# Performance work log

Hardware: AMD Instinct MI355X
Metric: run time of the kernel (lower is better)

The kernel has to match this reference:

```python
import jax, jax.numpy as jnp
import numpy as np

DIM = 2240; HEADS = 20; HD = 112
B = 1; F = 8; H = 16; W = 28; S = F * H * W; ENC = 300
HID = int(3.0 * DIM)  # 6720
EPS_LN = 1e-6; EPS_RMS = 1e-5


def setup_inputs():
    ks = iter(jax.random.split(jax.random.key(0), 64))
    nrm = lambda shape, s=1.0: jax.random.normal(next(ks), shape, jnp.float32) * s
    wsc = 0.02
    inp = dict(
        hidden_states=nrm((B, S, DIM)),
        encoder_hidden_states=nrm((B, ENC, DIM)),
        timestep=nrm((B, 6 * DIM), 0.1),
        freqs_cos=nrm((1, S, 1, HD)),
        freqs_sin=nrm((1, S, 1, HD)),
        scale_shift_table=nrm((6, DIM), 1.0 / np.sqrt(DIM)),
    )
    for p in ("a1", "a2"):
        inp[p + "_qw"] = nrm((DIM, DIM), wsc); inp[p + "_qb"] = jnp.zeros((DIM,), jnp.float32)
        inp[p + "_kw"] = nrm((DIM, DIM), wsc); inp[p + "_kb"] = jnp.zeros((DIM,), jnp.float32)
        inp[p + "_vw"] = nrm((DIM, DIM), wsc); inp[p + "_vb"] = jnp.zeros((DIM,), jnp.float32)
        inp[p + "_nq"] = jnp.ones((DIM,), jnp.float32)
        inp[p + "_nk"] = jnp.ones((DIM,), jnp.float32)
        inp[p + "_ow"] = nrm((DIM, DIM), wsc); inp[p + "_ob"] = jnp.zeros((DIM,), jnp.float32)
    inp["ff_inv_w"] = nrm((1, 1, DIM, 2 * HID), wsc)
    inp["ff_inv_b"] = jnp.zeros((2 * HID,), jnp.float32)
    inp["ff_depth_w"] = nrm((3, 3, 1, 2 * HID), wsc)
    inp["ff_depth_b"] = jnp.zeros((2 * HID,), jnp.float32)
    inp["ff_point_w"] = nrm((1, 1, HID, DIM), wsc)
    inp["ff_temp_w"] = nrm((3, 1, DIM, DIM), wsc)
    inp["frames"] = F; inp["height"] = H; inp["width"] = W
    return inp


def _ln(x):  # LayerNorm, no affine (elementwise_affine=False)
    m = jnp.mean(x, -1, keepdims=True)
    v = jnp.mean((x - m) ** 2, -1, keepdims=True)
    return (x - m) * jax.lax.rsqrt(v + EPS_LN)


def _rms(x, w):  # rms_norm_across_heads on full inner dim
    return x * jax.lax.rsqrt(jnp.mean(x * x, -1, keepdims=True) + EPS_RMS) * w


def _rope(x, cos, sin):  # interleaved rotary as in SanaLinearAttnProcessor3_0
    x1, x2 = x[..., 0::2], x[..., 1::2]
    c, s = cos[..., 0::2], sin[..., 1::2]
    out = jnp.stack([x1 * c - x2 * s, x1 * s + x2 * c], axis=-1)
    return out.reshape(x.shape)


def _conv(x, k, padding, groups=1):
    return jax.lax.conv_general_dilated(
        x, k, (1, 1), padding,
        dimension_numbers=("NHWC", "HWIO", "NHWC"),
        feature_group_count=groups)


def _linear_attn(x, qw, qb, kw, kb, vw, vb, nq, nk, ow, ob, cos, sin):
    b, s, _ = x.shape
    q = jax.nn.relu(_rms(x @ qw + qb, nq)).reshape(b, s, HEADS, HD)
    k = jax.nn.relu(_rms(x @ kw + kb, nk)).reshape(b, s, HEADS, HD)
    v = (x @ vw + vb).reshape(b, s, HEADS, HD)
    qr, kr = _rope(q, cos, sin), _rope(k, cos, sin)
    ksum = jnp.sum(k, axis=1)                             # [b,h,d] (un-rotated)
    denom = jnp.einsum("bhd,bshd->bsh", ksum, q) + 1e-15  # z^{-1}
    scores = jnp.einsum("bshe,bshd->bhed", v, kr)         # [b,h,dv,d]
    out = jnp.einsum("bhed,bshd->bshe", scores, qr) / denom[..., None]
    return out.reshape(b, s, HEADS * HD) @ ow + ob


def _cross_attn(x, enc, qw, qb, kw, kb, vw, vb, nq, nk, ow, ob):
    b, s, _ = x.shape; t = enc.shape[1]
    q = _rms(x @ qw + qb, nq).reshape(b, s, HEADS, HD)
    k = _rms(enc @ kw + kb, nk).reshape(b, t, HEADS, HD)
    v = (enc @ vw + vb).reshape(b, t, HEADS, HD)
    logits = jnp.einsum("bshd,bthd->bhst", q, k) / np.sqrt(HD).astype(np.float32)
    attn = jax.nn.softmax(logits, axis=-1)
    out = jnp.einsum("bhst,bthd->bshd", attn, v).reshape(b, s, HEADS * HD)
    return out @ ow + ob


def _ff(x, inv_w, inv_b, depth_w, depth_b, point_w, temp_w, f, h, w):
    b = x.shape[0]
    y = x.reshape(b * f, h, w, DIM)
    y = jax.nn.silu(_conv(y, inv_w, "SAME") + inv_b)
    y = _conv(y, depth_w, "SAME", groups=2 * HID) + depth_b
    a, g = y[..., :HID], y[..., HID:]
    y = _conv(a * jax.nn.silu(g), point_w, "SAME")        # [bf,h,w,DIM]
    yt = y.reshape(b, f, h * w, DIM)                      # conv over frames axis
    yt = yt + _conv(yt, temp_w, ((1, 1), (0, 0)))
    return yt.reshape(b, f, h, w, DIM)


def reference(hidden_states, encoder_hidden_states, timestep, freqs_cos, freqs_sin,
              scale_shift_table,
              a1_qw, a1_qb, a1_kw, a1_kb, a1_vw, a1_vb, a1_nq, a1_nk, a1_ow, a1_ob,
              a2_qw, a2_qb, a2_kw, a2_kb, a2_vw, a2_vb, a2_nq, a2_nk, a2_ow, a2_ob,
              ff_inv_w, ff_inv_b, ff_depth_w, ff_depth_b, ff_point_w, ff_temp_w,
              frames, height, width):
    b = hidden_states.shape[0]
    mods = scale_shift_table[None] + timestep.reshape(b, 6, DIM)
    sh_msa, sc_msa, g_msa, sh_mlp, sc_mlp, g_mlp = jnp.split(mods, 6, axis=1)
    nh = _ln(hidden_states) * (1 + sc_msa) + sh_msa
    attn = _linear_attn(nh, a1_qw, a1_qb, a1_kw, a1_kb, a1_vw, a1_vb,
                        a1_nq, a1_nk, a1_ow, a1_ob, freqs_cos, freqs_sin)
    x = hidden_states + g_msa * attn
    x = x + _cross_attn(x, encoder_hidden_states, a2_qw, a2_qb, a2_kw, a2_kb,
                        a2_vw, a2_vb, a2_nq, a2_nk, a2_ow, a2_ob)
    nh = _ln(x) * (1 + sc_mlp) + sh_mlp
    ff = _ff(nh.reshape(b, frames, height, width, DIM),
             ff_inv_w, ff_inv_b, ff_depth_w, ff_depth_b, ff_point_w, ff_temp_w,
             frames, height, width)
    x = x + g_mlp * ff.reshape(b, frames * height * width, DIM)
    return x
```

## Files before the change

kernel.cpp:

```cpp
#include <hip/hip_runtime.h>

#define DIMC 2240
#define STOK 3584
#define ENCT 300
#define NH   20
#define HDIM 112
#define HID1 6720
#define HID2 13440
#define DD   (2240*2240)
#define SD   (3584*2240)

typedef short bf16x8 __attribute__((ext_vector_type(8)));
typedef float f32x4  __attribute__((ext_vector_type(4)));

__device__ __forceinline__ unsigned short f2bf(float f){
  unsigned int u = __float_as_uint(f);
  u += 0x7fffu + ((u >> 16) & 1u);
  return (unsigned short)(u >> 16);
}
__device__ __forceinline__ float bf2f(unsigned short h){
  return __uint_as_float(((unsigned int)h) << 16);
}
__device__ __forceinline__ void gl_lds16(const unsigned short* g, unsigned short* l){
  __builtin_amdgcn_global_load_lds(
      (const __attribute__((address_space(1))) unsigned int*)(const void*)g,
      (__attribute__((address_space(3))) unsigned int*)(void*)l, 16, 0, 0);
}

__global__ void cvt_k(const float4* __restrict__ src, ushort4* __restrict__ dst, int n4){
  int i = blockIdx.x*256 + threadIdx.x;
  if (i < n4){
    float4 v = src[i];
    ushort4 o; o.x = f2bf(v.x); o.y = f2bf(v.y); o.z = f2bf(v.z); o.w = f2bf(v.w);
    dst[i] = o;
  }
}

__global__ __launch_bounds__(256) void cvt_t_k(const float* __restrict__ src,
    unsigned short* __restrict__ dst, int rows, int ldsrc, int c0, int nc){
  __shared__ float tile[32][33];
  const int tx = threadIdx.x & 31, ty = threadIdx.x >> 5;
  const int colBase = blockIdx.x*32;
  #pragma unroll
  for (int i = 0; i < 4; ++i){
    int rr = blockIdx.y*32 + ty + i*8;
    int cc = colBase + tx;
    tile[ty + i*8][tx] = (cc < nc) ? src[(size_t)rr*ldsrc + c0 + cc] : 0.f;
  }
  __syncthreads();
  #pragma unroll
  for (int i = 0; i < 4; ++i){
    int n = colBase + ty + i*8;
    int k = blockIdx.y*32 + tx;
    dst[(size_t)n*rows + k] = f2bf(tile[tx][ty + i*8]);
  }
}

__global__ void pack3_k(float* __restrict__ dst, const float* __restrict__ b0,
    const float* __restrict__ b1, const float* __restrict__ b2, int nslots){
  int i = blockIdx.x*256 + threadIdx.x;
  if (i >= nslots*2304) return;
  int slot = i / 2304, d = i - slot*2304;
  const float* src = (slot == 0) ? b0 : ((slot == 1) ? b1 : b2);
  dst[i] = (d < 2240) ? src[d] : 0.f;
}

__global__ void mods_k(const float* __restrict__ sst, const float* __restrict__ ts, float* __restrict__ mods){
  int i = blockIdx.x*256 + threadIdx.x;
  if (i < 6*DIMC) mods[i] = sst[i] + ts[i];
}

__global__ __launch_bounds__(256) void ln_mod_k(const float* __restrict__ x,
    const float* __restrict__ mods, int shj, int scj, unsigned short* __restrict__ out)
{
  const int s = blockIdx.x;
  const float* row = x + (size_t)s*DIMC;
  const float* sh = mods + shj*DIMC;
  const float* sc = mods + scj*DIMC;
  float sum = 0.f, sq = 0.f;
  for (int d = threadIdx.x; d < DIMC; d += 256){ float v = row[d]; sum += v; sq += v*v; }
  #pragma unroll
  for (int o = 32; o; o >>= 1){ sum += __shfl_down(sum, o); sq += __shfl_down(sq, o); }
  __shared__ float sA[4], sB[4];
  int w = threadIdx.x >> 6, l = threadIdx.x & 63;
  if (!l){ sA[w] = sum; sB[w] = sq; }
  __syncthreads();
  sum = sA[0]+sA[1]+sA[2]+sA[3];
  sq  = sB[0]+sB[1]+sB[2]+sB[3];
  float mean = sum * (1.f/DIMC);
  float rs = rsqrtf(sq*(1.f/DIMC) - mean*mean + 1e-6f);
  unsigned short* orow = out + (size_t)s*DIMC;
  for (int d = threadIdx.x; d < DIMC; d += 256){
    float v = (row[d]-mean)*rs*(1.f + sc[d]) + sh[d];
    orow[d] = f2bf(v);
  }
}

template<int RELU, int ROPE>
__global__ __launch_bounds__(256) void rms_bf_k(unsigned short* __restrict__ x, const float* __restrict__ nw,
    const float* __restrict__ cosb, const float* __restrict__ sinb, unsigned short* __restrict__ xr)
{
  const int s = blockIdx.x;
  unsigned short* row = x + (size_t)s*DIMC;
  float sq = 0.f;
  for (int d = threadIdx.x; d < DIMC; d += 256){ float v = bf2f(row[d]); sq += v*v; }
  #pragma unroll
  for (int o = 32; o; o >>= 1) sq += __shfl_down(sq, o);
  __shared__ float sB[4];
  int w = threadIdx.x >> 6, l = threadIdx.x & 63;
  if (!l) sB[w] = sq;
  __syncthreads();
  sq = sB[0]+sB[1]+sB[2]+sB[3];
  float rs = rsqrtf(sq*(1.f/DIMC) + 1e-5f);
  if constexpr (!ROPE){
    for (int d = threadIdx.x; d < DIMC; d += 256){
      float v = bf2f(row[d])*rs*nw[d];
      if (RELU) v = fmaxf(v, 0.f);
      row[d] = f2bf(v);
    }
  } else {
    for (int p = threadIdx.x; p < DIMC/2; p += 256){
      int d0 = 2*p, d1 = d0+1;
      float v0 = bf2f(row[d0])*rs*nw[d0];
      float v1 = bf2f(row[d1])*rs*nw[d1];
      if (RELU){ v0 = fmaxf(v0,0.f); v1 = fmaxf(v1,0.f); }
      row[d0] = f2bf(v0); row[d1] = f2bf(v1);
      int j0 = d0 % HDIM;
      float c  = cosb[(size_t)s*HDIM + j0];
      float sn = sinb[(size_t)s*HDIM + j0 + 1];
      xr[(size_t)s*DIMC + d0] = f2bf(v0*c - v1*sn);
      xr[(size_t)s*DIMC + d1] = f2bf(v0*sn + v1*c);
    }
  }
}

template<int EPI>
__global__ __launch_bounds__(256) void gemm_bt(
  const unsigned short* __restrict__ A, const unsigned short* __restrict__ Bt,
  const float* __restrict__ bias, float* __restrict__ Cf, unsigned short* __restrict__ Cb,
  const float* __restrict__ res, const float* __restrict__ gate,
  int M, int N, int K, int ldc, int PW)
{
  __shared__ __align__(16) unsigned short Al[128*64];
  __shared__ __align__(16) unsigned short Bl[128*64];
  const int gx = gridDim.x, gy = gridDim.y;
  const int nwg = gx*gy;
  const int orig = blockIdx.y*gx + blockIdx.x;
  const int qq = nwg >> 3, rr = nwg & 7;
  const int xcd = orig & 7, li = orig >> 3;
  const int wg = (xcd < rr ? xcd*(qq+1) : rr*(qq+1) + (xcd-rr)*qq) + li;
  const int ppw = gy*PW;
  const int panel = wg / ppw, rm = wg - panel*ppw;
  const int mrow = rm / PW;
  const int m0 = mrow*128;
  const int n0 = (panel*PW + (rm - mrow*PW))*128;

  const int t = threadIdx.x, lane = t & 63, w = t >> 6;
  const int wr = w >> 1, wc = w & 1;
  const int l16 = lane & 15, lk = lane >> 4;

  const int lr8 = lane >> 3;
  const int sc  = (lane & 7) ^ lr8;
  const unsigned short* Aps[4];
  const unsigned short* Bps[4];
  #pragma unroll
  for (int i = 0; i < 4; ++i){
    int ar = m0 + w*32 + i*8 + lr8;
    int br = n0 + w*32 + i*8 + lr8;
    Aps[i] = A  + (size_t)min(ar, M-1)*K + sc*8;
    Bps[i] = Bt + (size_t)br*K + sc*8;
  }
  unsigned short* Ad = Al + w*2048;
  unsigned short* Bd = Bl + w*2048;

  f32x4 acc[4][4] = {};
  for (int k0 = 0; k0 < K; k0 += 64){
    __syncthreads();
    #pragma unroll
    for (int i = 0; i < 4; ++i){
      gl_lds16(Aps[i] + k0, Ad + i*512);
      gl_lds16(Bps[i] + k0, Bd + i*512);
    }
    __syncthreads();
    #pragma unroll
    for (int kk = 0; kk < 2; ++kk){
      bf16x8 af[4], bfr[4];
      const int chb = (kk*4 + lk) ^ (l16 & 7);
      #pragma unroll
      for (int m = 0; m < 4; ++m)
        af[m] = *reinterpret_cast<const bf16x8*>(Al + (wr*64 + m*16 + l16)*64 + chb*8);
      #pragma unroll
      for (int n = 0; n < 4; ++n)
        bfr[n] = *reinterpret_cast<const bf16x8*>(Bl + (wc*64 + n*16 + l16)*64 + chb*8);
      #pragma unroll
      for (int m = 0; m < 4; ++m)
        #pragma unroll
        for (int n = 0; n < 4; ++n)
          acc[m][n] = __builtin_amdgcn_mfma_f32_16x16x32_bf16(af[m], bfr[n], acc[m][n], 0, 0, 0);
    }
  }

  const int rb = m0 + wr*64 + lk*4;
  const int cb = n0 + wc*64 + l16;
  #pragma unroll
  for (int m = 0; m < 4; ++m){
    #pragma unroll
    for (int r = 0; r < 4; ++r){
      int row = rb + m*16 + r;
      if (row >= M) continue;
      #pragma unroll
      for (int n = 0; n < 4; ++n){
        int col = cb + n*16;
        if (col >= N) continue;
        float v = acc[m][n][r];
        float bv = bias ? bias[col] : 0.f;
        if constexpr (EPI == 6){
          int slot = col / 2304;
          int d = col - slot*2304;
          if (d < 2240)
            Cb[(size_t)slot*ldc + (size_t)row*2240 + d] = f2bf(v + bv);
        } else {
          size_t idx = (size_t)row*ldc + col;
          if constexpr (EPI == 0){ Cf[idx] = v + bv; }
          else if constexpr (EPI == 1){ float u = v + bv; Cb[idx] = f2bf(u / (1.f + __expf(-u))); }
          else if constexpr (EPI == 2){ Cb[idx] = f2bf(v + bv); }
          else if constexpr (EPI == 3){ float u = res[idx] + gate[col]*(v + bv); Cf[idx] = u; Cb[idx] = f2bf(u); }
          else if constexpr (EPI == 4){ Cf[idx] = res[idx] + v + bv; }
          else { Cf[idx] += v; }
        }
      }
    }
  }
}

__global__ void colsum_k(const unsigned short* __restrict__ k, float* __restrict__ kpart){
  int d = blockIdx.x*256 + threadIdx.x;
  if (d >= DIMC) return;
  int ch = blockIdx.y, s0 = ch*128;
  float acc = 0.f;
  for (int s = s0; s < s0+128; ++s) acc += bf2f(k[(size_t)s*DIMC + d]);
  kpart[(size_t)ch*DIMC + d] = acc;
}
__global__ void ksumred_k(const float* __restrict__ kpart, float* __restrict__ ksum){
  int d = blockIdx.x*256 + threadIdx.x;
  if (d >= DIMC) return;
  float a = 0.f;
  for (int c = 0; c < 28; ++c) a += kpart[(size_t)c*DIMC + d];
  ksum[d] = a;
}
__global__ __launch_bounds__(256) void denom_k(const unsigned short* __restrict__ q,
    const float* __restrict__ ksum, float* __restrict__ denom)
{
  int s = blockIdx.x; int w = threadIdx.x >> 6, l = threadIdx.x & 63;
  for (int h = w; h < NH; h += 4){
    const unsigned short* qb = q + (size_t)s*DIMC + h*HDIM;
    const float* kb = ksum + h*HDIM;
    float v = bf2f(qb[l])*kb[l];
    if (l < 48) v += bf2f(qb[64+l])*kb[64+l];
    #pragma unroll
    for (int o = 32; o; o >>= 1) v += __shfl_down(v, o);
    if (!l) denom[s*NH + h] = v + 1e-15f;
  }
}

#define SLSC 136
__device__ __forceinline__ int sc_idx(int e, int s){
  return e*SLSC + (s ^ (((e >> 3) & 7) << 3));
}
__global__ __launch_bounds__(256) void scores_k(const unsigned short* __restrict__ v,
    const unsigned short* __restrict__ kr, float* __restrict__ part)
{
  const int h = blockIdx.x, ch = blockIdx.y;
  __shared__ __align__(16) unsigned short Vt[112*SLSC];
  __shared__ __align__(16) unsigned short Kt[112*SLSC];
  const int t = threadIdx.x, lane = t & 63, w = t >> 6;
  const int l16 = lane & 15, lk = lane >> 4;
  const int sbase = ch*128;

  for (int p = t; p < 1792; p += 256){
    int s = p / 14, oc = (p % 14) * 8;
    bf16x8 vv = *reinterpret_cast<const bf16x8*>(v  + (size_t)(sbase+s)*DIMC + h*HDIM + oc);
    bf16x8 kk = *reinterpret_cast<const bf16x8*>(kr + (size_t)(sbase+s)*DIMC + h*HDIM + oc);
    #pragma unroll
    for (int j = 0; j < 8; ++j){
      Vt[sc_idx(oc+j, s)] = (unsigned short)vv[j];
      Kt[sc_idx(oc+j, s)] = (unsigned short)kk[j];
    }
  }
  __syncthreads();

  f32x4 acc[2][7] = {};
  #pragma unroll
  for (int ks = 0; ks < 4; ++ks){
    const int sf = ks*32 + lk*8;
    bf16x8 bfrg[7];
    #pragma unroll
    for (int nt = 0; nt < 7; ++nt){
      int d = nt*16 + l16;
      bfrg[nt] = *reinterpret_cast<const bf16x8*>(&Kt[d*SLSC + (sf ^ (((d >> 3) & 7) << 3))]);
    }
    #pragma unroll
    for (int mi = 0; mi < 2; ++mi){
      int mt = w + mi*4;
      if (mt < 7){
        int e = mt*16 + l16;
        bf16x8 afrg = *reinterpret_cast<const bf16x8*>(&Vt[e*SLSC + (sf ^ (((e >> 3) & 7) << 3))]);
        #pragma unroll
        for (int nt = 0; nt < 7; ++nt)
          acc[mi][nt] = __builtin_amdgcn_mfma_f32_16x16x32_bf16(afrg, bfrg[nt], acc[mi][nt], 0, 0, 0);
      }
    }
  }

  float* pout = part + ((size_t)ch*NH + h)*12544;
  #pragma unroll
  for (int mi = 0; mi < 2; ++mi){
    int mt = w + mi*4;
    if (mt >= 7) continue;
    #pragma unroll
    for (int nt = 0; nt < 7; ++nt)
      #pragma unroll
      for (int r = 0; r < 4; ++r)
        pout[(size_t)(mt*16 + lk*4 + r)*HDIM + nt*16 + l16] = acc[mi][nt][r];
  }
}
__global__ void scred_k(const float* __restrict__ part, unsigned short* __restrict__ sc){
  int i = blockIdx.x*256 + threadIdx.x;
  if (i >= NH*HDIM*HDIM) return;
  float a = 0.f;
  #pragma unroll
  for (int c = 0; c < 28; ++c) a += part[(size_t)c*(NH*HDIM*HDIM) + i];
  sc[i] = f2bf(a);
}

__global__ __launch_bounds__(256) void linout_k(const unsigned short* __restrict__ qr,
    const unsigned short* __restrict__ scores, const float* __restrict__ denom,
    unsigned short* __restrict__ out)
{
  const int h = blockIdx.y;
  const int t = threadIdx.x, lane = t & 63, w = t >> 6;
  const int l16 = lane & 15, lk = lane >> 4;
  const int s0 = blockIdx.x*64 + w*16;
  const unsigned short* qrow = qr + (size_t)(s0 + l16)*DIMC + h*HDIM;
  const unsigned short* sb = scores + (size_t)h*12544;
  f32x4 acc[7] = {};
  #pragma unroll
  for (int ks = 0; ks < 4; ++ks){
    int d0 = ks*32 + lk*8;
    bf16x8 a = {};
    if (d0 < HDIM) a = *reinterpret_cast<const bf16x8*>(qrow + d0);
    #pragma unroll
    for (int nt = 0; nt < 7; ++nt){
      bf16x8 b = {};
      if (d0 < HDIM) b = *reinterpret_cast<const bf16x8*>(sb + (size_t)(nt*16 + l16)*HDIM + d0);
      acc[nt] = __builtin_amdgcn_mfma_f32_16x16x32_bf16(a, b, acc[nt], 0, 0, 0);
    }
  }
  #pragma unroll
  for (int r = 0; r < 4; ++r){
    int s = s0 + lk*4 + r;
    float dn = 1.f / denom[(size_t)s*NH + h];
    #pragma unroll
    for (int nt = 0; nt < 7; ++nt)
      out[(size_t)s*DIMC + h*HDIM + nt*16 + l16] = f2bf(acc[nt][r]*dn);
  }
}

__global__ __launch_bounds__(256) void xattn_k(
    const unsigned short* __restrict__ q,
    const unsigned short* __restrict__ k2,
    const unsigned short* __restrict__ v2,
    unsigned short* __restrict__ outb)
{
  const int h = blockIdx.y;
  const int w = threadIdx.x >> 6, lane = threadIdx.x & 63;
  const int l16 = lane & 15, lk = lane >> 4;
  const float scale = 0.09449111825230679f;

  __shared__ __align__(16) unsigned short Kl[64][136];
  __shared__ __align__(16) unsigned short Vl[112][72];
  __shared__ __align__(16) unsigned short Pl[4][16][72];

  bf16x8 qf[4];
  const unsigned short* qbase = q + (size_t)(blockIdx.x*64 + w*16 + l16)*DIMC + h*HDIM;
  #pragma unroll
  for (int c = 0; c < 4; ++c){
    int d0 = c*32 + lk*8;
    bf16x8 z = {};
    qf[c] = (d0 < HDIM) ? *reinterpret_cast<const bf16x8*>(qbase + d0) : z;
  }

  f32x4 lg[5][4] = {};
  #pragma unroll
  for (int c = 0; c < 5; ++c){
    const int kbase = c*64;
    const int nk = (c == 4) ? (ENCT - 256) : 64;
    __syncthreads();
    #pragma unroll
    for (int it = 0; it < 4; ++it){
      int li = it*256 + threadIdx.x;
      int key = li >> 4, d0 = (li & 15) << 3;
      uint4 val = make_uint4(0u,0u,0u,0u);
      if (key < nk && d0 < HDIM)
        val = *reinterpret_cast<const uint4*>(k2 + (size_t)(kbase+key)*DIMC + h*HDIM + d0);
      *reinterpret_cast<uint4*>(&Kl[key][d0]) = val;
    }
    __syncthreads();
    #pragma unroll
    for (int nt = 0; nt < 4; ++nt){
      #pragma unroll
      for (int ks = 0; ks < 4; ++ks){
        bf16x8 kf = *reinterpret_cast<const bf16x8*>(&Kl[nt*16 + l16][ks*32 + lk*8]);
        lg[c][nt] = __builtin_amdgcn_mfma_f32_16x16x32_bf16(qf[ks], kf, lg[c][nt], 0, 0, 0);
      }
    }
  }

  float mx[4] = {-3e38f, -3e38f, -3e38f, -3e38f};
  #pragma unroll
  for (int c = 0; c < 5; ++c)
    #pragma unroll
    for (int nt = 0; nt < 4; ++nt){
      bool valid = (c*64 + nt*16 + l16) < ENCT;
      #pragma unroll
      for (int r = 0; r < 4; ++r){
        float v = valid ? lg[c][nt][r]*scale : -3e38f;
        lg[c][nt][r] = v;
        mx[r] = fmaxf(mx[r], v);
      }
    }
  #pragma unroll
  for (int o = 1; o < 16; o <<= 1)
    #pragma unroll
    for (int r = 0; r < 4; ++r) mx[r] = fmaxf(mx[r], __shfl_xor(mx[r], o));
  float sm[4] = {0.f, 0.f, 0.f, 0.f};
  #pragma unroll
  for (int c = 0; c < 5; ++c)
    #pragma unroll
    for (int nt = 0; nt < 4; ++nt)
      #pragma unroll
      for (int r = 0; r < 4; ++r){
        float e = __expf(lg[c][nt][r] - mx[r]);
        lg[c][nt][r] = e;
        sm[r] += e;
      }
  #pragma unroll
  for (int o = 1; o < 16; o <<= 1)
    #pragma unroll
    for (int r = 0; r < 4; ++r) sm[r] += __shfl_xor(sm[r], o);
  float inv[4];
  #pragma unroll
  for (int r = 0; r < 4; ++r) inv[r] = 1.f / sm[r];

  f32x4 oacc[7] = {};
  #pragma unroll
  for (int c = 0; c < 5; ++c){
    const int kbase = c*64;
    const int nk = (c == 4) ? (ENCT - 256) : 64;
    __syncthreads();
    #pragma unroll
    for (int it = 0; it < 4; ++it){
      int li = it*256 + threadIdx.x;
      if (li < 896){
        int key = li/14, d0 = (li%14)*8;
        if (key < nk){
          bf16x8 vv = *reinterpret_cast<const bf16x8*>(v2 + (size_t)(kbase+key)*DIMC + h*HDIM + d0);
          #pragma unroll
          for (int j = 0; j < 8; ++j) Vl[d0+j][key] = (unsigned short)vv[j];
        } else {
          #pragma unroll
          for (int j = 0; j < 8; ++j) Vl[d0+j][key] = 0;
        }
      }
    }
    #pragma unroll
    for (int nt = 0; nt < 4; ++nt)
      #pragma unroll
      for (int r = 0; r < 4; ++r)
        Pl[w][lk*4 + r][nt*16 + l16] = f2bf(lg[c][nt][r]);
    __syncthreads();
    #pragma unroll
    for (int ks = 0; ks < 2; ++ks){
      bf16x8 pf = *reinterpret_cast<const bf16x8*>(&Pl[w][l16][ks*32 + lk*8]);
      #pragma unroll
      for (int n = 0; n < 7; ++n){
        bf16x8 vf = *reinterpret_cast<const bf16x8*>(&Vl[n*16 + l16][ks*32 + lk*8]);
        oacc[n] = __builtin_amdgcn_mfma_f32_16x16x32_bf16(pf, vf, oacc[n], 0, 0, 0);
      }
    }
  }

  const int orow = blockIdx.x*64 + w*16 + lk*4;
  #pragma unroll
  for (int n = 0; n < 7; ++n)
    #pragma unroll
    for (int r = 0; r < 4; ++r)
      outb[(size_t)(orow + r)*DIMC + h*HDIM + n*16 + l16] = f2bf(oacc[n][r]*inv[r]);
}

__global__ __launch_bounds__(256) void dw_k(const unsigned short* __restrict__ y1,
    const float* __restrict__ dw, const float* __restrict__ db, unsigned short* __restrict__ y2)
{
  int c = (blockIdx.y*256 + threadIdx.x)*2;
  if (c >= HID1) return;
  int bx = blockIdx.x;
  int ww = bx % 28;
  int yt = (bx / 28) & 3;
  int f  = bx / 112;
  int y0 = yt*4;

  float wa[9][2], wg[9][2];
  #pragma unroll
  for (int tp = 0; tp < 9; ++tp){
    float2 va = *reinterpret_cast<const float2*>(dw + tp*HID2 + c);
    float2 vg = *reinterpret_cast<const float2*>(dw + tp*HID2 + c + HID1);
    wa[tp][0] = va.x; wa[tp][1] = va.y;
    wg[tp][0] = vg.x; wg[tp][1] = vg.y;
  }
  float2 ba = *reinterpret_cast<const float2*>(db + c);
  float2 bg = *reinterpret_cast<const float2*>(db + c + HID1);
  float a0[4], a1[4], g0[4], g1[4];
  #pragma unroll
  for (int r = 0; r < 4; ++r){ a0[r] = ba.x; a1[r] = ba.y; g0[r] = bg.x; g1[r] = bg.y; }

  #pragma unroll
  for (int dy6 = 0; dy6 < 6; ++dy6){
    int y = y0 - 1 + dy6;
    if ((unsigned)y >= 16u) continue;
    #pragma unroll
    for (int dx = 0; dx < 3; ++dx){
      int x = ww + dx - 1;
      if ((unsigned)x >= 28u) continue;
      size_t base = ((size_t)(f*16 + y)*28 + x)*HID2;
      unsigned int a01 = *reinterpret_cast<const unsigned int*>(y1 + base + c);
      unsigned int g01 = *reinterpret_cast<const unsigned int*>(y1 + base + c + HID1);
      float fa0 = bf2f((unsigned short)(a01 & 0xffffu));
      float fa1 = bf2f((unsigned short)(a01 >> 16));
      float fg0 = bf2f((unsigned short)(g01 & 0xffffu));
      float fg1 = bf2f((unsigned short)(g01 >> 16));
      #pragma unroll
      for (int r = 0; r < 4; ++r){
        int kdy = dy6 - r;
        if (kdy < 0 || kdy > 2) continue;
        int tp = kdy*3 + dx;
        a0[r] += fa0*wa[tp][0]; a1[r] += fa1*wa[tp][1];
        g0[r] += fg0*wg[tp][0]; g1[r] += fg1*wg[tp][1];
      }
    }
  }
  #pragma unroll
  for (int r = 0; r < 4; ++r){
    float s0 = g0[r] / (1.f + __expf(-g0[r]));
    float s1 = g1[r] / (1.f + __expf(-g1[r]));
    int pos = (f*16 + y0 + r)*28 + ww;
    unsigned int o = (unsigned int)f2bf(a0[r]*s0) | ((unsigned int)f2bf(a1[r]*s1) << 16);
    *reinterpret_cast<unsigned int*>(y2 + (size_t)pos*HID1 + c) = o;
  }
}

__global__ void final_k(const float* __restrict__ x2, const unsigned short* __restrict__ y3,
    const float* __restrict__ tc, const float* __restrict__ mods, float* __restrict__ out)
{
  int i = blockIdx.x*256 + threadIdx.x;
  if (i >= SD) return;
  int d = i % DIMC;
  out[i] = x2[i] + mods[5*DIMC + d]*(bf2f(y3[i]) + tc[i]);
}

extern "C" void kernel_launch(void* const* d_in, const int* in_sizes, int n_in,
                              void* d_out, int out_size, void* d_ws, size_t ws_size,
                              hipStream_t stream)
{
  const float* hid   = (const float*)d_in[0];
  const float* enc   = (const float*)d_in[1];
  const float* tstep = (const float*)d_in[2];
  const float* fcos  = (const float*)d_in[3];
  const float* fsin  = (const float*)d_in[4];
  const float* sst   = (const float*)d_in[5];
  const float *a1_qw=(const float*)d_in[6],  *a1_qb=(const float*)d_in[7];
  const float *a1_kw=(const float*)d_in[8],  *a1_kb=(const float*)d_in[9];
  const float *a1_vw=(const float*)d_in[10], *a1_vb=(const float*)d_in[11];
  const float *a1_nq=(const float*)d_in[12], *a1_nk=(const float*)d_in[13];
  const float *a1_ow=(const float*)d_in[14], *a1_ob=(const float*)d_in[15];
  const float *a2_qw=(const float*)d_in[16], *a2_qb=(const float*)d_in[17];
  const float *a2_kw=(const float*)d_in[18], *a2_kb=(const float*)d_in[19];
  const float *a2_vw=(const float*)d_in[20], *a2_vb=(const float*)d_in[21];
  const float *a2_nq=(const float*)d_in[22], *a2_nk=(const float*)d_in[23];
  const float *a2_ow=(const float*)d_in[24], *a2_ob=(const float*)d_in[25];
  const float *ff_inv_w=(const float*)d_in[26], *ff_inv_b=(const float*)d_in[27];
  const float *ff_dw=(const float*)d_in[28], *ff_db=(const float*)d_in[29];
  const float *ff_pw=(const float*)d_in[30];
  const float *ff_tw=(const float*)d_in[31];
  float* out = (float*)d_out;

  const size_t SLOTB = (size_t)SD*2;
  char* ws = (char*)d_ws;
  size_t off = 0;
  auto alloc = [&](size_t n){ void* p = ws + off; off += (n + 255) & ~(size_t)255; return p; };

  char* P = (char*)alloc(6*SLOTB);
  float* x1    = (float*)alloc((size_t)SD*4);
  unsigned short* nh2b = (unsigned short*)alloc(SLOTB);
  float* x2    = (float*)alloc((size_t)SD*4);
  unsigned short* k2b = (unsigned short*)alloc((size_t)ENCT*DIMC*2);
  unsigned short* v2b = (unsigned short*)alloc((size_t)ENCT*DIMC*2);
  unsigned short* encb = (unsigned short*)alloc((size_t)ENCT*DIMC*2);
  float* modsb = (float*)alloc(6*DIMC*4);
  float* ksum  = (float*)alloc(DIMC*4);
  float* kpart = (float*)alloc((size_t)28*DIMC*4);
  float* denom = (float*)alloc((size_t)STOK*NH*4);
  unsigned short* scorb = (unsigned short*)alloc((size_t)NH*HDIM*HDIM*2);
  float* bias3 = (float*)alloc(3*2304*4);
  unsigned short* Wbig = (unsigned short*)alloc((size_t)6912*DIMC*2);

  unsigned short* P0 = (unsigned short*)P;
  unsigned short* P1 = (unsigned short*)(P + 1*SLOTB);
  unsigned short* P2 = (unsigned short*)(P + 2*SLOTB);
  unsigned short* P3 = (unsigned short*)(P + 3*SLOTB);
  unsigned short* P4 = (unsigned short*)(P + 4*SLOTB);
  unsigned short* P5 = (unsigned short*)(P + 5*SLOTB);
  unsigned short* nhb = P0;
  unsigned short* y1b = P0;
  unsigned short* y2b = (unsigned short*)x1;
  unsigned short* y3b = P0;
  float* tc = (float*)(P + 1*SLOTB);
  float* spart = (float*)P1;

  auto cvt = [&](const float* s, unsigned short* d, size_t n){
    int n4 = (int)(n/4);
    cvt_k<<<dim3((n4+255)/256), 256, 0, stream>>>((const float4*)s, (ushort4*)d, n4);
  };
  auto cvtT = [&](const float* s, unsigned short* d, int rows, int ldsrc, int c0, int nc, int ncPad){
    cvt_t_k<<<dim3(ncPad/32, rows/32), 256, 0, stream>>>(s, d, rows, ldsrc, c0, nc);
  };
  auto gemm_grid = [&](int M, int Npad){ return dim3(Npad/128, (M+127)/128); };

  mods_k<<<dim3((6*DIMC+255)/256), 256, 0, stream>>>(sst, tstep, modsb);
  cvt(enc, encb, (size_t)ENCT*DIMC);

  ln_mod_k<<<dim3(STOK), 256, 0, stream>>>(hid, modsb, 0, 1, nhb);
  pack3_k<<<dim3((3*2304+255)/256), 256, 0, stream>>>(bias3, a1_qb, a1_kb, a1_vb, 3);
  cvtT(a1_qw, Wbig + (size_t)0*2304*DIMC, DIMC, DIMC, 0, DIMC, 2304);
  cvtT(a1_kw, Wbig + (size_t)1*2304*DIMC, DIMC, DIMC, 0, DIMC, 2304);
  cvtT(a1_vw, Wbig + (size_t)2*2304*DIMC, DIMC, DIMC, 0, DIMC, 2304);
  gemm_bt<6><<<gemm_grid(STOK, 6912), 256, 0, stream>>>(nhb, Wbig, bias3, nullptr, P1,
                                                        nullptr, nullptr, STOK, 6912, DIMC, SD, 6);
  rms_bf_k<1,1><<<dim3(STOK), 256, 0, stream>>>(P1, a1_nq, fcos, fsin, P4);
  rms_bf_k<1,1><<<dim3(STOK), 256, 0, stream>>>(P2, a1_nk, fcos, fsin, P5);
  colsum_k<<<dim3(9, 28), 256, 0, stream>>>(P2, kpart);
  ksumred_k<<<dim3(9), 256, 0, stream>>>(kpart, ksum);
  denom_k<<<dim3(STOK), 256, 0, stream>>>(P1, ksum, denom);
  scores_k<<<dim3(NH, 28), 256, 0, stream>>>(P3, P5, spart);
  scred_k<<<dim3((NH*HDIM*HDIM+255)/256), 256, 0, stream>>>(spart, scorb);
  linout_k<<<dim3(STOK/64, NH), 256, 0, stream>>>(P4, scorb, denom, P1);
  dim3 gMN = gemm_grid(STOK, 2304);
  cvtT(a1_ow, Wbig, DIMC, DIMC, 0, DIMC, 2304);
  gemm_bt<3><<<gMN, 256, 0, stream>>>(P1, Wbig, a1_ob, x1, P2, hid, modsb + 2*DIMC, STOK, DIMC, DIMC, DIMC, 6);

  cvtT(a2_qw, Wbig, DIMC, DIMC, 0, DIMC, 2304);
  gemm_bt<2><<<gMN, 256, 0, stream>>>(P2, Wbig, a2_qb, nullptr, P3, nullptr, nullptr, STOK, DIMC, DIMC, DIMC, 6);
  pack3_k<<<dim3((2*2304+255)/256), 256, 0, stream>>>(bias3, a2_kb, a2_vb, a2_vb, 2);
  cvtT(a2_kw, Wbig + (size_t)0*2304*DIMC, DIMC, DIMC, 0, DIMC, 2304);
  cvtT(a2_vw, Wbig + (size_t)1*2304*DIMC, DIMC, DIMC, 0, DIMC, 2304);
  gemm_bt<6><<<gemm_grid(ENCT, 4608), 256, 0, stream>>>(encb, Wbig, bias3, nullptr, k2b,
                                                        nullptr, nullptr, ENCT, 4608, DIMC, ENCT*DIMC, 6);
  rms_bf_k<0,0><<<dim3(STOK), 256, 0, stream>>>(P3, a2_nq, nullptr, nullptr, nullptr);
  rms_bf_k<0,0><<<dim3(ENCT), 256, 0, stream>>>(k2b, a2_nk, nullptr, nullptr, nullptr);
  xattn_k<<<dim3(STOK/64, NH), 256, 0, stream>>>(P3, k2b, v2b, P4);
  cvtT(a2_ow, Wbig, DIMC, DIMC, 0, DIMC, 2304);
  gemm_bt<4><<<gMN, 256, 0, stream>>>(P4, Wbig, a2_ob, x2, nullptr, x1, nullptr, STOK, DIMC, DIMC, DIMC, 6);

  ln_mod_k<<<dim3(STOK), 256, 0, stream>>>(x2, modsb, 3, 4, nh2b);
  for (int q = 0; q < 2; ++q){
    int c0 = q*6720;
    cvtT(ff_inv_w, Wbig, DIMC, HID2, c0, 6720, 6912);
    gemm_bt<1><<<gemm_grid(STOK, 6912), 256, 0, stream>>>(nh2b, Wbig, ff_inv_b + c0, nullptr, y1b + c0,
                                                          nullptr, nullptr, STOK, 6720, DIMC, HID2, 6);
  }
  dw_k<<<dim3(896, 14), 256, 0, stream>>>(y1b, ff_dw, ff_db, y2b);
  cvtT(ff_pw, Wbig, HID1, DIMC, 0, DIMC, 2304);
  gemm_bt<2><<<gMN, 256, 0, stream>>>(y2b, Wbig, nullptr, nullptr, y3b,
                                      nullptr, nullptr, STOK, DIMC, HID1, DIMC, 2);
  cvtT(ff_tw + (size_t)DD, Wbig, DIMC, DIMC, 0, DIMC, 2304);
  gemm_bt<0><<<gMN, 256, 0, stream>>>(y3b, Wbig, nullptr, tc, nullptr, nullptr, nullptr, STOK, DIMC, DIMC, DIMC, 6);
  dim3 gT = gemm_grid(3136, 2304);
  cvtT(ff_tw, Wbig, DIMC, DIMC, 0, DIMC, 2304);
  gemm_bt<5><<<gT, 256, 0, stream>>>(y3b, Wbig, nullptr, tc + (size_t)448*DIMC, nullptr, nullptr, nullptr, 3136, DIMC, DIMC, DIMC, 6);
  cvtT(ff_tw + (size_t)2*DD, Wbig, DIMC, DIMC, 0, DIMC, 2304);
  gemm_bt<5><<<gT, 256, 0, stream>>>(y3b + (size_t)448*DIMC, Wbig, nullptr, tc, nullptr, nullptr, nullptr, 3136, DIMC, DIMC, DIMC, 6);

  final_k<<<dim3((SD+255)/256), 256, 0, stream>>>(x2, y3b, tc, modsb, out);
}
```

Before: 1.533 ms.

## Pipeline GEMM K-loop with 4-stage LDS ring buffer and async prefetch

Replaces the single-buffer GEMM main loop, which synchronized twice per 64-wide K step, with a 4-slot LDS ring of 32-wide K tiles. Loads run three tiles ahead, and the loop waits with an explicit vmcnt and one barrier per iteration. The LDS layout and swizzle change to a paired-row layout, and MFMA issue gets raised priority via setprio. The goal is to hide global-to-LDS latency behind MFMA work, at the cost of doubled LDS use (64KB per block), which may lower occupancy.

```diff
diff --git a/kernel.cpp b/kernel.cpp
--- a/kernel.cpp
+++ b/kernel.cpp
@@ -141,8 +141,8 @@
   const float* __restrict__ res, const float* __restrict__ gate,
   int M, int N, int K, int ldc, int PW)
 {
-  __shared__ __align__(16) unsigned short Al[128*64];
-  __shared__ __align__(16) unsigned short Bl[128*64];
+  __shared__ __align__(16) unsigned short Al[4*4096];
+  __shared__ __align__(16) unsigned short Bl[4*4096];
   const int gx = gridDim.x, gy = gridDim.y;
   const int nwg = gx*gy;
   const int orig = blockIdx.y*gx + blockIdx.x;
@@ -159,45 +159,62 @@
   const int wr = w >> 1, wc = w & 1;
   const int l16 = lane & 15, lk = lane >> 4;
 
-  const int lr8 = lane >> 3;
-  const int sc  = (lane & 7) ^ lr8;
-  const unsigned short* Aps[4];
-  const unsigned short* Bps[4];
-  #pragma unroll
-  for (int i = 0; i < 4; ++i){
-    int ar = m0 + w*32 + i*8 + lr8;
-    int br = n0 + w*32 + i*8 + lr8;
-    Aps[i] = A  + (size_t)min(ar, M-1)*K + sc*8;
-    Bps[i] = Bt + (size_t)br*K + sc*8;
-  }
-  unsigned short* Ad = Al + w*2048;
-  unsigned short* Bd = Bl + w*2048;
+  const int lr  = lane >> 3;
+  const int hl  = (lane >> 2) & 1;
+  const int cg  = (lane & 3) ^ (lr & 3);
+  const unsigned short* Asrc[2];
+  const unsigned short* Bsrc[2];
+  #pragma unroll
+  for (int i = 0; i < 2; ++i){
+    int ar = m0 + i*64 + w*16 + lr*2 + hl;
+    int br = n0 + i*64 + w*16 + lr*2 + hl;
+    Asrc[i] = A  + (size_t)min(ar, M-1)*K + cg*8;
+    Bsrc[i] = Bt + (size_t)br*K + cg*8;
+  }
+  const int ldsOff = w*512;
+
+  const int NT = K >> 5;
+  #pragma unroll
+  for (int p = 0; p < 3; ++p){
+    #pragma unroll
+    for (int i = 0; i < 2; ++i) gl_lds16(Asrc[i] + p*32, Al + p*4096 + i*2048 + ldsOff);
+    #pragma unroll
+    for (int i = 0; i < 2; ++i) gl_lds16(Bsrc[i] + p*32, Bl + p*4096 + i*2048 + ldsOff);
+  }
 
   f32x4 acc[4][4] = {};
-  for (int k0 = 0; k0 < K; k0 += 64){
-    __syncthreads();
-    #pragma unroll
-    for (int i = 0; i < 4; ++i){
-      gl_lds16(Aps[i] + k0, Ad + i*512);
-      gl_lds16(Bps[i] + k0, Bd + i*512);
-    }
-    __syncthreads();
-    #pragma unroll
-    for (int kk = 0; kk < 2; ++kk){
-      bf16x8 af[4], bfr[4];
-      const int chb = (kk*4 + lk) ^ (l16 & 7);
-      #pragma unroll
-      for (int m = 0; m < 4; ++m)
-        af[m] = *reinterpret_cast<const bf16x8*>(Al + (wr*64 + m*16 + l16)*64 + chb*8);
-      #pragma unroll
-      for (int n = 0; n < 4; ++n)
-        bfr[n] = *reinterpret_cast<const bf16x8*>(Bl + (wc*64 + n*16 + l16)*64 + chb*8);
-      #pragma unroll
-      for (int m = 0; m < 4; ++m)
-        #pragma unroll
-        for (int n = 0; n < 4; ++n)
-          acc[m][n] = __builtin_amdgcn_mfma_f32_16x16x32_bf16(af[m], bfr[n], acc[m][n], 0, 0, 0);
-    }
+  for (int u = 0; u < NT; ++u){
+    asm volatile("s_waitcnt vmcnt(8)" ::: "memory");
+    __builtin_amdgcn_s_barrier();
+    __builtin_amdgcn_sched_barrier(0);
+    {
+      int us = u + 3; if (us > NT-1) us = NT-1;
+      int bs = (u + 3) & 3;
+      #pragma unroll
+      for (int i = 0; i < 2; ++i) gl_lds16(Asrc[i] + us*32, Al + bs*4096 + i*2048 + ldsOff);
+      #pragma unroll
+      for (int i = 0; i < 2; ++i) gl_lds16(Bsrc[i] + us*32, Bl + bs*4096 + i*2048 + ldsOff);
+    }
+    const unsigned short* Ab = Al + (u & 3)*4096;
+    const unsigned short* Bb = Bl + (u & 3)*4096;
+    bf16x8 af[4], bfr[4];
+    #pragma unroll
+    for (int mt = 0; mt < 4; ++mt){
+      int r = wr*64 + mt*16 + l16;
+      af[mt] = *reinterpret_cast<const bf16x8*>(Ab + (r>>1)*64 + (r&1)*32 + ((lk ^ ((r>>1)&3))<<3));
+    }
+    #pragma unroll
+    for (int nt = 0; nt < 4; ++nt){
+      int r = wc*64 + nt*16 + l16;
+      bfr[nt] = *reinterpret_cast<const bf16x8*>(Bb + (r>>1)*64 + (r&1)*32 + ((lk ^ ((r>>1)&3))<<3));
+    }
+    __builtin_amdgcn_s_setprio(1);
+    #pragma unroll
+    for (int mt = 0; mt < 4; ++mt)
+      #pragma unroll
+      for (int nt = 0; nt < 4; ++nt)
+        acc[mt][nt] = __builtin_amdgcn_mfma_f32_16x16x32_bf16(af[mt], bfr[nt], acc[mt][nt], 0, 0, 0);
+    __builtin_amdgcn_s_setprio(0);
   }
 
   const int rb = m0 + wr*64 + lk*4;
```

Measured after the change: 1.706 ms. +11.2%, slower.
